# Optimization experiments

Measured on AMD Instinct MI355X. Metric: run time of the kernel, lower is better.

Reference implementation:

```python
import math
import jax, jax.numpy as jnp
import numpy as np

HEAD_DIM = 64


def skew(X):
    # X: (B, M, L). Pad M+1 zeros on last dim, flatten, drop last M, reshape.
    # Shifts row i right by i -> aligns relative positions (adaptive-span trick).
    B, M, L = X.shape
    X = jnp.pad(X, ((0, 0), (0, 0), (0, M + 1)))  # (B, M, L+M+1)
    X = X.reshape(B, -1)[:, :-M].reshape(B, M, M + L)
    return X


def setup_inputs() -> dict:
    key = jax.random.key(0)
    k1, k2, k3, k4 = jax.random.split(key, 4)
    BH, M, D, LIM = 16, 2048, HEAD_DIM, 2048
    return {
        "query": jax.random.normal(k1, (BH, M, D), jnp.float32),
        "key": jax.random.normal(k2, (BH, M, D), jnp.float32),
        "value": jax.random.normal(k3, (BH, M, D), jnp.float32),
        "key_pe": jax.random.normal(k4, (1, D, LIM), jnp.float32),
    }


def reference(query, key, value, key_pe):
    M = query.shape[1]
    Lk = key.shape[1]
    neg_inf = jnp.float32(float("-inf"))
    # causal mask: -inf strictly above diagonal, last M rows
    mask_causal = jnp.triu(jnp.full((Lk, Lk), neg_inf, dtype=query.dtype), k=1)[-M:]
    # content scores: (BH, M, Lk)
    attn = jnp.einsum("bmd,bld->bml", query, key)
    L_size = attn.shape[-1]
    # relative-position scores via skew trick
    attn_pos = jnp.einsum("bmd,xdl->bml", query, key_pe[:, :, -L_size:])
    attn_pos = skew(attn_pos)[:, :, -L_size - 1:-1]
    attn = (attn + attn_pos + mask_causal) / math.sqrt(HEAD_DIM)
    attn = jax.nn.softmax(attn, axis=-1)
    out = jnp.einsum("bml,bld->bmd", attn, value)
    return out  # aux_loss is the constant 0 in the original module
```

## Files before the change

### kernel.cpp

```cpp
#include <hip/hip_runtime.h>
#include <hip/hip_bf16.h>

typedef __attribute__((ext_vector_type(8))) short short8;
typedef __attribute__((ext_vector_type(4))) float f32x4;

#define MFMA16(A, B, C) __builtin_amdgcn_mfma_f32_16x16x32_bf16((A), (B), (C), 0, 0, 0)

#define GL16(gp, lp) __builtin_amdgcn_global_load_lds( \
    (const __attribute__((address_space(1))) void*)(gp), \
    (__attribute__((address_space(3))) void*)(lp), 16, 0, 0)

extern "C" __device__ float __ocml_native_exp2_f32(float);
#define EXP2(x) __ocml_native_exp2_f32(x)

__device__ __forceinline__ unsigned short bfbits(float f) {
  return __builtin_bit_cast(unsigned short, (__bf16)f);
}

constexpr int BH = 16;
constexpr int Mn = 2048;
constexpr int Dn = 64;
constexpr int LIMn = 2048;
constexpr size_t KF_SHORTS = (size_t)BH * 32 * 8 * 512;
constexpr size_t PE_JROWS = 132;
constexpr size_t PEF_SHORTS = PE_JROWS * 2 * 512;
constexpr int PART_SLOT = 4224;
constexpr int SLOTS_PER_HEAD = 72;

__device__ __forceinline__ int part_offs(int mt) {
  return (mt < 16) ? 2 * (mt - 8) : (mt < 24 ? 16 + 3 * (mt - 16) : 40 + 4 * (mt - 24));
}


__global__ void prep_all(const float* __restrict__ K, const float* __restrict__ V,
                         const float* __restrict__ PE,
                         unsigned short* __restrict__ Kf, unsigned short* __restrict__ Vf,
                         unsigned short* __restrict__ PEf) {
  __shared__ float tA[64 * 64];
  __shared__ float tB[64 * 64];
  const int b = blockIdx.x, tid = threadIdx.x;
  const int w = tid >> 6, lane = tid & 63, g = lane >> 4, q15 = lane & 15;

  if (b < 512) {
    const int bh = b >> 5, lt = b & 31;
    const float* Ks = K + ((size_t)bh * Mn + lt * 64) * Dn;
    const float* Vs = V + ((size_t)bh * Mn + lt * 64) * Dn;
    const int row = tid >> 2, c0 = (tid & 3) * 16;
#pragma unroll
    for (int i = 0; i < 4; ++i) {
      *(float4*)&tA[row * 64 + c0 + 4 * i] = ((const float4*)(Ks + (size_t)row * 64 + c0))[i];
      *(float4*)&tB[row * 64 + c0 + 4 * i] = ((const float4*)(Vs + (size_t)row * 64 + c0))[i];
    }
    __syncthreads();
#pragma unroll
    for (int i = 0; i < 2; ++i) {
      const int f = 2 * w + i, nt = f >> 1, s = f & 1;
      short8 uk, uv;
#pragma unroll
      for (int jj = 0; jj < 8; ++jj) {
        uk[jj] = (short)bfbits(tA[(nt * 16 + q15) * 64 + s * 32 + g * 8 + jj]);
        uv[jj] = (short)bfbits(tB[(s * 32 + g * 8 + jj) * 64 + nt * 16 + q15]);
      }
      const size_t base = ((size_t)(bh * 32 + lt) * 8 + f) * 512 + lane * 8;
      *(short8*)&Kf[base] = uk;
      *(short8*)&Vf[base] = uv;
    }
  } else {
    const int pb = b - 512;
    const int c0 = pb * 64;
    const int d = tid >> 2, cc = (tid & 3) * 16;
#pragma unroll
    for (int i = 0; i < 16; ++i) {
      const int cx = c0 + cc + i;
      tA[(cc + i) * 64 + d] = (cx < LIMn) ? PE[(size_t)d * LIMn + cx] : 0.0f;
    }
    __syncthreads();
#pragma unroll
    for (int s = 0; s < 2; ++s) {
      short8 uu;
#pragma unroll
      for (int jj = 0; jj < 8; ++jj)
        uu[jj] = (short)bfbits(tA[(w * 16 + q15) * 64 + s * 32 + g * 8 + jj]);
      *(short8*)&PEf[((size_t)(4 * pb + w) * 2 + s) * 512 + lane * 8] = uu;
    }
  }
}


__launch_bounds__(256)
__global__ void stair_main(const float* __restrict__ Qg,
                           const unsigned short* __restrict__ Kf,
                           const unsigned short* __restrict__ Vf,
                           const unsigned short* __restrict__ PEf,
                           float* __restrict__ Og,
                           float* __restrict__ Part,
                           int split) {
  __shared__ __align__(16) unsigned short Kbuf[2][2][4096];
  __shared__ __align__(16) unsigned short Vbuf[2][2][4096];
  __shared__ __align__(16) unsigned short Plds[4][2048];

  const int tid = threadIdx.x;
  const int w = tid >> 6, lane = tid & 63, g = lane >> 4, q15 = lane & 15;
  const int bid = blockIdx.x;

  int bh, mt, chunk, t0, t1, nch;
  bh = bid & 15;
  if (split) {
    const int u = bid >> 4;
    if (u < 32)      { mt = 31 - (u >> 2); chunk = u & 3; }
    else if (u < 56) { const int v = u - 32, q = v / 3; mt = 23 - q; chunk = v - q * 3; }
    else if (u < 72) { const int v = u - 56; mt = 15 - (v >> 1); chunk = v & 1; }
    else             { mt = 7 - (u - 72); chunk = 0; }
    t0 = chunk * 8;
    t1 = (t0 + 8 < mt + 1) ? (t0 + 8) : (mt + 1);
    nch = (mt + 8) >> 3;
  } else {
    mt = 31 - (bid >> 4); chunk = 0; t0 = 0; t1 = mt + 1; nch = 1;
  }
  const int m0w = mt * 64 + w * 16;
  const int jb0 = 127 - 4 * mt - w;

  const float* Qb = Qg + (size_t)bh * Mn * Dn;
  float* Ob = Og + (size_t)bh * Mn * Dn;

  short8 aq[2];
  {
    const float* qp = Qb + (size_t)(m0w + q15) * Dn;
#pragma unroll
    for (int s = 0; s < 2; ++s) {
      const float4* p = (const float4*)(qp + s * 32 + g * 8);
      float4 f0 = p[0], f1 = p[1];
      short8 a;
      a[0]=(short)bfbits(f0.x); a[1]=(short)bfbits(f0.y); a[2]=(short)bfbits(f0.z); a[3]=(short)bfbits(f0.w);
      a[4]=(short)bfbits(f1.x); a[5]=(short)bfbits(f1.y); a[6]=(short)bfbits(f1.z); a[7]=(short)bfbits(f1.w);
      aq[s] = a;
    }
  }

  float mrun[4], lp[4];
  f32x4 o[4] = {};
#pragma unroll
  for (int r = 0; r < 4; ++r) { mrun[r] = -1e30f; lp[r] = 0.0f; }

  auto STAGE1 = [&](int b, int slot, int t) {
    const size_t toff = ((size_t)(bh * 32 + t) * 8) * 512;
#pragma unroll
    for (int i = 0; i < 2; ++i) {
      const int f = 2 * w + i;
      const size_t off = toff + (size_t)f * 512 + lane * 8;
      GL16(&Kf[off], &Kbuf[b][slot][f * 512]);
      GL16(&Vf[off], &Vbuf[b][slot][f * 512]);
    }
  };

  auto PV = [&](const float sv[4][4], int cur, int slot, int smax) {
#pragma unroll
    for (int nt = 0; nt < 4; ++nt)
#pragma unroll
      for (int r = 0; r < 4; ++r) {
        const int rw = g * 4 + r;
        Plds[w][slot * 1024 + ((rw * 64 + nt * 16 + q15) ^ ((rw & 7) << 3))] = bfbits(sv[nt][r]);
      }
    short8 pa[2];
#pragma unroll
    for (int s = 0; s < 2; ++s)
      if (s <= smax)
        pa[s] = *(short8*)&Plds[w][slot * 1024 + ((q15 * 64 + s * 32 + g * 8) ^ ((q15 & 7) << 3))];
#pragma unroll
    for (int s = 0; s < 2; ++s)
      if (s <= smax)
#pragma unroll
        for (int nt = 0; nt < 4; ++nt) {
          short8 bfr = *(const short8*)&Vbuf[cur][slot][(nt * 2 + s) * 512 + lane * 8];
          o[nt] = MFMA16(pa[s], bfr, o[nt]);
        }
  };

  auto SOFTMAX2 = [&](float svA[4][4], float svB[4][4]) {
    float lmax[4];
#pragma unroll
    for (int r = 0; r < 4; ++r) {
      float a = fmaxf(fmaxf(svA[0][r], svA[1][r]), fmaxf(svA[2][r], svA[3][r]));
      float b = fmaxf(fmaxf(svB[0][r], svB[1][r]), fmaxf(svB[2][r], svB[3][r]));
      lmax[r] = fmaxf(a, b);
    }
    const bool fast = __all((lmax[0] <= mrun[0] + 8.f) & (lmax[1] <= mrun[1] + 8.f) &
                            (lmax[2] <= mrun[2] + 8.f) & (lmax[3] <= mrun[3] + 8.f));
    if (!fast) {
#pragma unroll
      for (int r = 0; r < 4; ++r) {
        float mx = lmax[r];
        mx = fmaxf(mx, __shfl_xor(mx, 1));
        mx = fmaxf(mx, __shfl_xor(mx, 2));
        mx = fmaxf(mx, __shfl_xor(mx, 4));
        mx = fmaxf(mx, __shfl_xor(mx, 8));
        const float mn = fmaxf(mrun[r], mx);
        const float alpha = EXP2((mrun[r] - mn) * 1.44269504f);
        mrun[r] = mn;
        lp[r] *= alpha;
        o[0][r] *= alpha; o[1][r] *= alpha; o[2][r] *= alpha; o[3][r] *= alpha;
      }
    }
#pragma unroll
    for (int nt = 0; nt < 4; ++nt)
#pragma unroll
      for (int r = 0; r < 4; ++r) {
        svA[nt][r] = EXP2((svA[nt][r] - mrun[r]) * 1.44269504f);
        svB[nt][r] = EXP2((svB[nt][r] - mrun[r]) * 1.44269504f);
      }
#pragma unroll
    for (int r = 0; r < 4; ++r)
      lp[r] += ((svA[0][r] + svA[1][r]) + (svA[2][r] + svA[3][r])) +
               ((svB[0][r] + svB[1][r]) + (svB[2][r] + svB[3][r]));
  };

  auto PAIRF = [&](int t, int cur) {
    const int jbA = jb0 + 4 * t;
    const int jbB = jbA + 4;

    short8 peA[2][5], peB[2][5];
#pragma unroll
    for (int s = 0; s < 2; ++s)
#pragma unroll
      for (int uu = 0; uu < 5; ++uu) {
        peA[s][uu] = *(const short8*)&PEf[((size_t)(jbA + uu) * 2 + s) * 512 + lane * 8];
        peB[s][uu] = *(const short8*)&PEf[((size_t)(jbB + uu) * 2 + s) * 512 + lane * 8];
      }

    f32x4 qkA[4] = {}, qkB[4] = {};
#pragma unroll
    for (int s = 0; s < 2; ++s)
#pragma unroll
      for (int nt = 0; nt < 4; ++nt) {
        short8 ba = *(const short8*)&Kbuf[cur][0][(nt * 2 + s) * 512 + lane * 8];
        qkA[nt] = MFMA16(aq[s], ba, qkA[nt]);
        short8 bb = *(const short8*)&Kbuf[cur][1][(nt * 2 + s) * 512 + lane * 8];
        qkB[nt] = MFMA16(aq[s], bb, qkB[nt]);
      }

    f32x4 evA[5] = {};
#pragma unroll
    for (int s = 0; s < 2; ++s)
#pragma unroll
      for (int uu = 0; uu < 5; ++uu) evA[uu] = MFMA16(aq[s], peA[s][uu], evA[uu]);

    float svA[4][4], svB[4][4];
#pragma unroll
    for (int nt = 0; nt < 4; ++nt)
#pragma unroll
      for (int r = 0; r < 4; ++r) {
        const int rw = g * 4 + r;
        const int srcLane = (lane & 48) | ((q15 + 15 - rw) & 15);
        const bool cond = (((q15 + rw + 1) & 15) > rw);
        const float sel = cond ? evA[nt + 1][r] : evA[nt][r];
        svA[nt][r] = (qkA[nt][r] + __shfl(sel, srcLane, 64)) * 0.125f;
      }

    f32x4 evB[5] = {};
#pragma unroll
    for (int s = 0; s < 2; ++s)
#pragma unroll
      for (int uu = 0; uu < 5; ++uu) evB[uu] = MFMA16(aq[s], peB[s][uu], evB[uu]);

#pragma unroll
    for (int nt = 0; nt < 4; ++nt)
#pragma unroll
      for (int r = 0; r < 4; ++r) {
        const int rw = g * 4 + r;
        const int srcLane = (lane & 48) | ((q15 + 15 - rw) & 15);
        const bool cond = (((q15 + rw + 1) & 15) > rw);
        const float sel = cond ? evB[nt + 1][r] : evB[nt][r];
        svB[nt][r] = (qkB[nt][r] + __shfl(sel, srcLane, 64)) * 0.125f;
      }

    SOFTMAX2(svA, svB);
    PV(svA, cur, 0, 1);
    PV(svB, cur, 1, 1);
  };

  auto PAIRD = [&](int t, int cur) {
    const int jbA = jb0 + 4 * t;
    const int jbB = jbA + 4;
    const int ntmaxB = w;
    const int u5B = w + 2;
    const int smaxB = w >> 1;

    short8 peA[2][5], peB[2][5];
#pragma unroll
    for (int s = 0; s < 2; ++s)
#pragma unroll
      for (int uu = 0; uu < 5; ++uu) {
        peA[s][uu] = *(const short8*)&PEf[((size_t)(jbA + uu) * 2 + s) * 512 + lane * 8];
        if (uu < u5B)
          peB[s][uu] = *(const short8*)&PEf[((size_t)(jbB + uu) * 2 + s) * 512 + lane * 8];
      }

    f32x4 qkA[4] = {}, qkB[4] = {};
#pragma unroll
    for (int s = 0; s < 2; ++s)
#pragma unroll
      for (int nt = 0; nt < 4; ++nt) {
        short8 ba = *(const short8*)&Kbuf[cur][0][(nt * 2 + s) * 512 + lane * 8];
        qkA[nt] = MFMA16(aq[s], ba, qkA[nt]);
        if (nt <= ntmaxB) {
          short8 bb = *(const short8*)&Kbuf[cur][1][(nt * 2 + s) * 512 + lane * 8];
          qkB[nt] = MFMA16(aq[s], bb, qkB[nt]);
        }
      }

    f32x4 evA[5] = {};
#pragma unroll
    for (int s = 0; s < 2; ++s)
#pragma unroll
      for (int uu = 0; uu < 5; ++uu) evA[uu] = MFMA16(aq[s], peA[s][uu], evA[uu]);

    float svA[4][4], svB[4][4];
#pragma unroll
    for (int nt = 0; nt < 4; ++nt)
#pragma unroll
      for (int r = 0; r < 4; ++r) {
        const int rw = g * 4 + r;
        const int srcLane = (lane & 48) | ((q15 + 15 - rw) & 15);
        const bool cond = (((q15 + rw + 1) & 15) > rw);
        const float sel = cond ? evA[nt + 1][r] : evA[nt][r];
        svA[nt][r] = (qkA[nt][r] + __shfl(sel, srcLane, 64)) * 0.125f;
        svB[nt][r] = -1e30f;
      }

    f32x4 evB[5] = {};
#pragma unroll
    for (int s = 0; s < 2; ++s)
#pragma unroll
      for (int uu = 0; uu < 5; ++uu)
        if (uu < u5B) evB[uu] = MFMA16(aq[s], peB[s][uu], evB[uu]);

#pragma unroll
    for (int nt = 0; nt < 4; ++nt)
      if (nt <= ntmaxB) {
#pragma unroll
        for (int r = 0; r < 4; ++r) {
          const int rw = g * 4 + r;
          const int srcLane = (lane & 48) | ((q15 + 15 - rw) & 15);
          const bool cond = (((q15 + rw + 1) & 15) > rw);
          const float sel = cond ? evB[nt + 1][r] : evB[nt][r];
          const float er = __shfl(sel, srcLane, 64);
          const int li = nt * 16 + q15;
          const bool masked = (li > w * 16 + rw);
          svB[nt][r] = masked ? -1e30f : (qkB[nt][r] + er) * 0.125f;
        }
      }

    SOFTMAX2(svA, svB);
    PV(svA, cur, 0, 1);
    PV(svB, cur, 1, smaxB);
  };

  auto SINGLE = [&](int t, int cur, bool diag) {
    const int jb = jb0 + 4 * t;
    const int ntmax = diag ? w : 3;
    const int u5 = diag ? (w + 2) : 5;
    const int smax = diag ? (w >> 1) : 1;

    short8 pe[2][5];
#pragma unroll
    for (int s = 0; s < 2; ++s)
#pragma unroll
      for (int uu = 0; uu < 5; ++uu)
        if (uu < u5)
          pe[s][uu] = *(const short8*)&PEf[((size_t)(jb + uu) * 2 + s) * 512 + lane * 8];

    f32x4 qk[4] = {};
#pragma unroll
    for (int s = 0; s < 2; ++s)
#pragma unroll
      for (int nt = 0; nt < 4; ++nt)
        if (nt <= ntmax) {
          short8 bfr = *(const short8*)&Kbuf[cur][0][(nt * 2 + s) * 512 + lane * 8];
          qk[nt] = MFMA16(aq[s], bfr, qk[nt]);
        }
    f32x4 ev[5] = {};
#pragma unroll
    for (int s = 0; s < 2; ++s)
#pragma unroll
      for (int uu = 0; uu < 5; ++uu)
        if (uu < u5) ev[uu] = MFMA16(aq[s], pe[s][uu], ev[uu]);

    float sv[4][4];
#pragma unroll
    for (int nt = 0; nt < 4; ++nt)
#pragma unroll
      for (int r = 0; r < 4; ++r) sv[nt][r] = -1e30f;
#pragma unroll
    for (int nt = 0; nt < 4; ++nt)
      if (nt <= ntmax) {
#pragma unroll
        for (int r = 0; r < 4; ++r) {
          const int rw = g * 4 + r;
          const int srcLane = (lane & 48) | ((q15 + 15 - rw) & 15);
          const bool cond = (((q15 + rw + 1) & 15) > rw);
          const float sel = cond ? ev[nt + 1][r] : ev[nt][r];
          const float er = __shfl(sel, srcLane, 64);
          const int li = nt * 16 + q15;
          const bool masked = diag && (li > w * 16 + rw);
          sv[nt][r] = masked ? -1e30f : (qk[nt][r] + er) * 0.125f;
        }
      }

    float lmax[4];
#pragma unroll
    for (int r = 0; r < 4; ++r)
      lmax[r] = fmaxf(fmaxf(sv[0][r], sv[1][r]), fmaxf(sv[2][r], sv[3][r]));
    const bool fast = __all((lmax[0] <= mrun[0] + 8.f) & (lmax[1] <= mrun[1] + 8.f) &
                            (lmax[2] <= mrun[2] + 8.f) & (lmax[3] <= mrun[3] + 8.f));
    if (!fast) {
#pragma unroll
      for (int r = 0; r < 4; ++r) {
        float mx = lmax[r];
        mx = fmaxf(mx, __shfl_xor(mx, 1));
        mx = fmaxf(mx, __shfl_xor(mx, 2));
        mx = fmaxf(mx, __shfl_xor(mx, 4));
        mx = fmaxf(mx, __shfl_xor(mx, 8));
        const float mn = fmaxf(mrun[r], mx);
        const float alpha = EXP2((mrun[r] - mn) * 1.44269504f);
        mrun[r] = mn;
        lp[r] *= alpha;
        o[0][r] *= alpha; o[1][r] *= alpha; o[2][r] *= alpha; o[3][r] *= alpha;
      }
    }
#pragma unroll
    for (int nt = 0; nt < 4; ++nt)
#pragma unroll
      for (int r = 0; r < 4; ++r)
        sv[nt][r] = EXP2((sv[nt][r] - mrun[r]) * 1.44269504f);
#pragma unroll
    for (int r = 0; r < 4; ++r)
      lp[r] += (sv[0][r] + sv[1][r]) + (sv[2][r] + sv[3][r]);
    PV(sv, cur, 0, smax);
  };

  {
    int cur = 0;
    int t = t0;
    const int n0 = (t1 - t0 >= 2) ? 2 : 1;
    STAGE1(0, 0, t0);
    if (n0 == 2) STAGE1(0, 1, t0 + 1);
    __syncthreads();
    while (t < t1) {
      const int n = (t1 - t >= 2) ? 2 : 1;
      const int rem = t1 - (t + n);
      const int nn = (rem >= 2) ? 2 : rem;
      if (nn > 0) {
        STAGE1(cur ^ 1, 0, t + n);
        if (nn == 2) STAGE1(cur ^ 1, 1, t + n + 1);
      }
      if (n == 2) {
        if (t + 1 == mt) PAIRD(t, cur);
        else PAIRF(t, cur);
      } else {
        SINGLE(t, cur, (t == mt));
      }
      if (nn > 0) __syncthreads();
      cur ^= 1;
      t += n;
    }
  }

  float lr[4];
#pragma unroll
  for (int r = 0; r < 4; ++r) {
    float s = lp[r];
    s += __shfl_xor(s, 1);
    s += __shfl_xor(s, 2);
    s += __shfl_xor(s, 4);
    s += __shfl_xor(s, 8);
    lr[r] = s;
  }

  if (nch == 1) {
#pragma unroll
    for (int nt = 0; nt < 4; ++nt)
#pragma unroll
      for (int r = 0; r < 4; ++r) {
        const int m = m0w + g * 4 + r;
        Ob[(size_t)m * Dn + nt * 16 + q15] = o[nt][r] / lr[r];
      }
  } else {
    float* ps = Part + ((size_t)bh * SLOTS_PER_HEAD + part_offs(mt) + chunk) * PART_SLOT;
#pragma unroll
    for (int nt = 0; nt < 4; ++nt)
#pragma unroll
      for (int r = 0; r < 4; ++r)
        ps[(w * 16 + g * 4 + r) * 64 + nt * 16 + q15] = o[nt][r];
#pragma unroll
    for (int r = 0; r < 4; ++r)
      if (q15 == g * 4 + r) {
        ps[4096 + w * 16 + q15] = mrun[r];
        ps[4160 + w * 16 + q15] = lr[r];
      }
  }
}


__launch_bounds__(256, 4)
__global__ void combine_parts(const float* __restrict__ Part, float* __restrict__ Og) {
  const int bid = blockIdx.x;
  const int bh = bid & 15;
  const int mt = 8 + (bid >> 4);
  const int nch = (mt + 8) >> 3;
  const float* base = Part + ((size_t)bh * SLOTS_PER_HEAD + part_offs(mt)) * PART_SLOT;
  const int tid = threadIdx.x;
  const int row = tid >> 2;
  const int qc = (tid & 3) * 16;

  float mstar = -1e30f;
#pragma unroll
  for (int cc = 0; cc < 4; ++cc)
    if (cc < nch) mstar = fmaxf(mstar, base[cc * PART_SLOT + 4096 + row]);
  float lsum = 0.f;
  f32x4 acc0 = {}, acc1 = {}, acc2 = {}, acc3 = {};
#pragma unroll
  for (int cc = 0; cc < 4; ++cc)
    if (cc < nch) {
      const float* ps = base + cc * PART_SLOT;
      const float sc = EXP2((ps[4096 + row] - mstar) * 1.44269504f);
      lsum += ps[4160 + row] * sc;
      const f32x4* op = (const f32x4*)&ps[row * 64 + qc];
      acc0 += op[0] * sc; acc1 += op[1] * sc; acc2 += op[2] * sc; acc3 += op[3] * sc;
    }
  const float inv = 1.f / lsum;
  float* dst = Og + ((size_t)bh * Mn + mt * 64 + row) * Dn + qc;
  *(f32x4*)&dst[0]  = acc0 * inv;
  *(f32x4*)&dst[4]  = acc1 * inv;
  *(f32x4*)&dst[8]  = acc2 * inv;
  *(f32x4*)&dst[12] = acc3 * inv;
}


constexpr int ESTRIDE = 84;

__launch_bounds__(256, 2)
__global__ void stair_attn_fb(const float* __restrict__ Qg,
                              const float* __restrict__ Kg,
                              const float* __restrict__ Vg,
                              const float* __restrict__ PEg,
                              float* __restrict__ Og) {
  __shared__ __align__(16) unsigned short Kb[64 * 64];
  __shared__ __align__(16) unsigned short Vt[64 * 64];
  __shared__ __align__(16) unsigned short Pb[128 * 64];
  __shared__ __align__(16) float Elds[4 * 16 * ESTRIDE];
  __shared__ __align__(16) unsigned short Plds[4 * 16 * 64];

  const int tid = threadIdx.x;
  const int w = tid >> 6;
  const int lane = tid & 63;
  const int g = lane >> 4;
  const int q15 = lane & 15;

  const int bid = blockIdx.x;
  const int bh = bid & 15;
  const int jid = bid >> 4;
  const int mt = (jid < 16) ? (2 * jid) : (63 - 2 * jid);
  const int m0 = mt * 64;

  const float* Qb = Qg + (size_t)bh * Mn * Dn;
  const float* Kbase = Kg + (size_t)bh * Mn * Dn;
  const float* Vbase = Vg + (size_t)bh * Mn * Dn;
  float* Ob = Og + (size_t)bh * Mn * Dn;

  short8 aq[2];
  {
    const float* qp = Qb + (size_t)(m0 + 16 * w + q15) * Dn;
#pragma unroll
    for (int s = 0; s < 2; ++s) {
      const float4* p = (const float4*)(qp + s * 32 + g * 8);
      float4 f0 = p[0], f1 = p[1];
      short8 a;
      a[0]=(short)bfbits(f0.x); a[1]=(short)bfbits(f0.y); a[2]=(short)bfbits(f0.z); a[3]=(short)bfbits(f0.w);
      a[4]=(short)bfbits(f1.x); a[5]=(short)bfbits(f1.y); a[6]=(short)bfbits(f1.z); a[7]=(short)bfbits(f1.w);
      aq[s] = a;
    }
  }

  float mrun[4], lrun[4];
  f32x4 o[4] = {};
#pragma unroll
  for (int r = 0; r < 4; ++r) { mrun[r] = -1e30f; lrun[r] = 0.0f; }

  const int ntiles = mt + 1;
  const int dso = g * 8;

  for (int t = 0; t < ntiles; ++t) {
    const int l0 = t * 64;
    __syncthreads();
    {
      const int l = tid >> 2;
      const int dq = (tid & 3) * 16;
      const float* kp = Kbase + (size_t)(l0 + l) * Dn + dq;
      short8 u0, u1;
      {
        float4 f = ((const float4*)kp)[0];
        u0[0]=(short)bfbits(f.x); u0[1]=(short)bfbits(f.y); u0[2]=(short)bfbits(f.z); u0[3]=(short)bfbits(f.w);
        f = ((const float4*)kp)[1];
        u0[4]=(short)bfbits(f.x); u0[5]=(short)bfbits(f.y); u0[6]=(short)bfbits(f.z); u0[7]=(short)bfbits(f.w);
        f = ((const float4*)kp)[2];
        u1[0]=(short)bfbits(f.x); u1[1]=(short)bfbits(f.y); u1[2]=(short)bfbits(f.z); u1[3]=(short)bfbits(f.w);
        f = ((const float4*)kp)[3];
        u1[4]=(short)bfbits(f.x); u1[5]=(short)bfbits(f.y); u1[6]=(short)bfbits(f.z); u1[7]=(short)bfbits(f.w);
      }
      const int swz = (l & 7) << 3;
      *(short8*)&Kb[(l * 64 + dq) ^ swz] = u0;
      *(short8*)&Kb[(l * 64 + dq + 8) ^ swz] = u1;
    }
    {
      const int lrow = lane;
      const int ds = w * 16;
      const float* vp = Vbase + (size_t)(l0 + lrow) * Dn + ds;
#pragma unroll
      for (int i = 0; i < 4; ++i) {
        float4 f = ((const float4*)vp)[i];
        int c0 = ds + 4 * i;
        Vt[((c0 + 0) * 64 + lrow) ^ (((c0 + 0) & 7) << 3)] = bfbits(f.x);
        Vt[((c0 + 1) * 64 + lrow) ^ (((c0 + 1) & 7) << 3)] = bfbits(f.y);
        Vt[((c0 + 2) * 64 + lrow) ^ (((c0 + 2) & 7) << 3)] = bfbits(f.z);
        Vt[((c0 + 3) * 64 + lrow) ^ (((c0 + 3) & 7) << 3)] = bfbits(f.w);
      }
    }
    {
      const int d = lane;
      const int cc = w * 32;
      const int cb = (2048 - 64) - m0 + l0;
      const float* pp = PEg + (size_t)d * LIMn + (cb + cc);
      if (cb + cc + 31 < LIMn) {
#pragma unroll
        for (int i = 0; i < 8; ++i) {
          float4 f = ((const float4*)pp)[i];
          int c0 = cc + 4 * i;
          Pb[((c0 + 0) * 64 + d) ^ (((c0 + 0) & 7) << 3)] = bfbits(f.x);
          Pb[((c0 + 1) * 64 + d) ^ (((c0 + 1) & 7) << 3)] = bfbits(f.y);
          Pb[((c0 + 2) * 64 + d) ^ (((c0 + 2) & 7) << 3)] = bfbits(f.z);
          Pb[((c0 + 3) * 64 + d) ^ (((c0 + 3) & 7) << 3)] = bfbits(f.w);
        }
      } else {
        for (int i = 0; i < 32; ++i) {
          int cabs = cb + cc + i;
          float f = (cabs < LIMn) ? pp[i] : 0.0f;
          int c0 = cc + i;
          Pb[(c0 * 64 + d) ^ ((c0 & 7) << 3)] = bfbits(f);
        }
      }
    }
    __syncthreads();

    f32x4 qk[4] = {};
#pragma unroll
    for (int s = 0; s < 2; ++s)
#pragma unroll
      for (int nt = 0; nt < 4; ++nt) {
        int l = nt * 16 + q15;
        short8 b = *(short8*)&Kb[(l * 64 + s * 32 + dso) ^ ((l & 7) << 3)];
        qk[nt] = MFMA16(aq[s], b, qk[nt]);
      }

    f32x4 ev[5] = {};
    const int ntb = 3 - w;
#pragma unroll
    for (int s = 0; s < 2; ++s)
#pragma unroll
      for (int u5 = 0; u5 < 5; ++u5) {
        int c = (ntb + u5) * 16 + q15;
        short8 b = *(short8*)&Pb[(c * 64 + s * 32 + dso) ^ ((c & 7) << 3)];
        ev[u5] = MFMA16(aq[s], b, ev[u5]);
      }
    float* Ew = Elds + w * 16 * ESTRIDE;
#pragma unroll
    for (int u5 = 0; u5 < 5; ++u5)
#pragma unroll
      for (int r = 0; r < 4; ++r)
        Ew[(g * 4 + r) * ESTRIDE + u5 * 16 + q15] = ev[u5][r];

    const bool diag = (t == ntiles - 1);
    float sv[4][4];
#pragma unroll
    for (int nt = 0; nt < 4; ++nt) {
      int li = nt * 16 + q15;
#pragma unroll
      for (int r = 0; r < 4; ++r) {
        int rw = g * 4 + r;
        float eread = Ew[rw * ESTRIDE + (15 - rw + li)];
        bool masked = diag && (li > (16 * w + rw));
        sv[nt][r] = masked ? -1e30f : (qk[nt][r] + eread) * 0.125f;
      }
    }

    float mnew[4], alpha[4];
#pragma unroll
    for (int r = 0; r < 4; ++r) {
      float mx = fmaxf(fmaxf(sv[0][r], sv[1][r]), fmaxf(sv[2][r], sv[3][r]));
      mx = fmaxf(mx, __shfl_xor(mx, 1));
      mx = fmaxf(mx, __shfl_xor(mx, 2));
      mx = fmaxf(mx, __shfl_xor(mx, 4));
      mx = fmaxf(mx, __shfl_xor(mx, 8));
      float mn = fmaxf(mrun[r], mx);
      alpha[r] = exp2f((mrun[r] - mn) * 1.44269504f);
      mnew[r] = mn;
      mrun[r] = mn;
    }
    float pexp[4][4];
#pragma unroll
    for (int nt = 0; nt < 4; ++nt)
#pragma unroll
      for (int r = 0; r < 4; ++r)
        pexp[nt][r] = exp2f((sv[nt][r] - mnew[r]) * 1.44269504f);
#pragma unroll
    for (int r = 0; r < 4; ++r) {
      float sum = (pexp[0][r] + pexp[1][r]) + (pexp[2][r] + pexp[3][r]);
      sum += __shfl_xor(sum, 1);
      sum += __shfl_xor(sum, 2);
      sum += __shfl_xor(sum, 4);
      sum += __shfl_xor(sum, 8);
      lrun[r] = lrun[r] * alpha[r] + sum;
      o[0][r] *= alpha[r];
      o[1][r] *= alpha[r];
      o[2][r] *= alpha[r];
      o[3][r] *= alpha[r];
    }

    unsigned short* Pw = Plds + w * 16 * 64;
#pragma unroll
    for (int nt = 0; nt < 4; ++nt)
#pragma unroll
      for (int r = 0; r < 4; ++r) {
        int rw = g * 4 + r;
        Pw[(rw * 64 + nt * 16 + q15) ^ ((rw & 7) << 3)] = bfbits(pexp[nt][r]);
      }
    short8 pa[2];
#pragma unroll
    for (int s = 0; s < 2; ++s)
      pa[s] = *(short8*)&Pw[(q15 * 64 + s * 32 + dso) ^ ((q15 & 7) << 3)];

#pragma unroll
    for (int s = 0; s < 2; ++s)
#pragma unroll
      for (int nt = 0; nt < 4; ++nt) {
        int d = nt * 16 + q15;
        short8 b = *(short8*)&Vt[(d * 64 + s * 32 + dso) ^ ((d & 7) << 3)];
        o[nt] = MFMA16(pa[s], b, o[nt]);
      }
  }

#pragma unroll
  for (int nt = 0; nt < 4; ++nt)
#pragma unroll
    for (int r = 0; r < 4; ++r) {
      int m = m0 + 16 * w + g * 4 + r;
      Ob[(size_t)m * Dn + nt * 16 + q15] = o[nt][r] / lrun[r];
    }
}


extern "C" void kernel_launch(void* const* d_in, const int* in_sizes, int n_in,
                              void* d_out, int out_size, void* d_ws, size_t ws_size,
                              hipStream_t stream) {
  (void)in_sizes; (void)n_in; (void)out_size;
  const float* Q  = (const float*)d_in[0];
  const float* K  = (const float*)d_in[1];
  const float* V  = (const float*)d_in[2];
  const float* PE = (const float*)d_in[3];
  float* Out = (float*)d_out;

  const size_t szK = KF_SHORTS * sizeof(unsigned short);
  const size_t szV = szK;
  const size_t szP = PEF_SHORTS * sizeof(unsigned short);
  const size_t szPart = (size_t)BH * SLOTS_PER_HEAD * PART_SLOT * 4;
  const size_t need1 = szK + szV + szP;
  const size_t need2 = need1 + szPart;

  if (ws_size >= need1) {
    unsigned short* Kf  = (unsigned short*)d_ws;
    unsigned short* Vf  = (unsigned short*)((char*)d_ws + szK);
    unsigned short* PEf = (unsigned short*)((char*)d_ws + szK + szV);
    float* Part = (float*)((char*)d_ws + need1);

    hipLaunchKernelGGL(prep_all, dim3(512 + 33), dim3(256), 0, stream, K, V, PE, Kf, Vf, PEf);
    if (ws_size >= need2) {
      hipLaunchKernelGGL(stair_main, dim3(BH * 80), dim3(256), 0, stream,
                         Q, Kf, Vf, PEf, Out, Part, 1);
      hipLaunchKernelGGL(combine_parts, dim3(BH * 24), dim3(256), 0, stream, Part, Out);
    } else {
      hipLaunchKernelGGL(stair_main, dim3(512), dim3(256), 0, stream,
                         Q, Kf, Vf, PEf, Out, (float*)d_ws, 0);
    }
  } else {
    hipLaunchKernelGGL(stair_attn_fb, dim3(512), dim3(256), 0, stream, Q, K, V, PE, Out);
  }
}
```

Measured before the change: 66.87 us.

## Fold softmax scale into Q, single-buffer V in LDS, shrink P scratch

Pre-multiplies Q by 0.125*log2(e) before the bf16 conversion, which removes the per-score scale and per-exp multiply and rescales the max-threshold to match. V is no longer double-buffered: it is loaded per step into one LDS buffer and waited on with an explicit vmcnt(0) before the PV MFMAs. The P staging area is cut to a 16x40 padded tile per half, and LDS use drops overall, which may allow more blocks per CU. The cost is that V loads are exposed within each step rather than prefetched a full iteration ahead, and the vmcnt(0) wait also drains the in-flight K prefetch.

```diff
diff --git a/kernel.cpp b/kernel.cpp
--- a/kernel.cpp
+++ b/kernel.cpp
@@ -26,6 +26,8 @@
 constexpr size_t PEF_SHORTS = PE_JROWS * 2 * 512;
 constexpr int PART_SLOT = 4224;
 constexpr int SLOTS_PER_HEAD = 72;
+constexpr float QSCALE = 0.125f * 1.44269504f;
+constexpr float THR = 11.5409504f;
 
 __device__ __forceinline__ int part_offs(int mt) {
   return (mt < 16) ? 2 * (mt - 8) : (mt < 24 ? 16 + 3 * (mt - 16) : 40 + 4 * (mt - 24));
@@ -96,8 +98,8 @@
                            float* __restrict__ Part,
                            int split) {
   __shared__ __align__(16) unsigned short Kbuf[2][2][4096];
-  __shared__ __align__(16) unsigned short Vbuf[2][2][4096];
-  __shared__ __align__(16) unsigned short Plds[4][2048];
+  __shared__ __align__(16) unsigned short Vbuf[2][4096];
+  __shared__ __align__(16) unsigned short Plds[4][640];
 
   const int tid = threadIdx.x;
   const int w = tid >> 6, lane = tid & 63, g = lane >> 4, q15 = lane & 15;
@@ -122,6 +124,7 @@
 
   const float* Qb = Qg + (size_t)bh * Mn * Dn;
   float* Ob = Og + (size_t)bh * Mn * Dn;
+  unsigned short* Pw = Plds[w];
 
   short8 aq[2];
   {
@@ -131,8 +134,10 @@
       const float4* p = (const float4*)(qp + s * 32 + g * 8);
       float4 f0 = p[0], f1 = p[1];
       short8 a;
-      a[0]=(short)bfbits(f0.x); a[1]=(short)bfbits(f0.y); a[2]=(short)bfbits(f0.z); a[3]=(short)bfbits(f0.w);
-      a[4]=(short)bfbits(f1.x); a[5]=(short)bfbits(f1.y); a[6]=(short)bfbits(f1.z); a[7]=(short)bfbits(f1.w);
+      a[0]=(short)bfbits(f0.x*QSCALE); a[1]=(short)bfbits(f0.y*QSCALE);
+      a[2]=(short)bfbits(f0.z*QSCALE); a[3]=(short)bfbits(f0.w*QSCALE);
+      a[4]=(short)bfbits(f1.x*QSCALE); a[5]=(short)bfbits(f1.y*QSCALE);
+      a[6]=(short)bfbits(f1.z*QSCALE); a[7]=(short)bfbits(f1.w*QSCALE);
       aq[s] = a;
     }
   }
@@ -142,36 +147,41 @@
 #pragma unroll
   for (int r = 0; r < 4; ++r) { mrun[r] = -1e30f; lp[r] = 0.0f; }
 
-  auto STAGE1 = [&](int b, int slot, int t) {
+  auto STAGEK = [&](int b, int slot, int t) {
     const size_t toff = ((size_t)(bh * 32 + t) * 8) * 512;
 #pragma unroll
     for (int i = 0; i < 2; ++i) {
       const int f = 2 * w + i;
-      const size_t off = toff + (size_t)f * 512 + lane * 8;
-      GL16(&Kf[off], &Kbuf[b][slot][f * 512]);
-      GL16(&Vf[off], &Vbuf[b][slot][f * 512]);
+      GL16(&Kf[toff + (size_t)f * 512 + lane * 8], &Kbuf[b][slot][f * 512]);
     }
   };
-
-  auto PV = [&](const float sv[4][4], int cur, int slot, int smax) {
-#pragma unroll
-    for (int nt = 0; nt < 4; ++nt)
-#pragma unroll
-      for (int r = 0; r < 4; ++r) {
-        const int rw = g * 4 + r;
-        Plds[w][slot * 1024 + ((rw * 64 + nt * 16 + q15) ^ ((rw & 7) << 3))] = bfbits(sv[nt][r]);
-      }
+  auto STAGEV = [&](int slot, int t) {
+    const size_t toff = ((size_t)(bh * 32 + t) * 8) * 512;
+#pragma unroll
+    for (int i = 0; i < 2; ++i) {
+      const int f = 2 * w + i;
+      GL16(&Vf[toff + (size_t)f * 512 + lane * 8], &Vbuf[slot][f * 512]);
+    }
+  };
+
+  auto PV = [&](const float sv[4][4], int slot, int smax) {
     short8 pa[2];
 #pragma unroll
+    for (int h = 0; h < 2; ++h)
+      if (h <= smax) {
+#pragma unroll
+        for (int nt2 = 0; nt2 < 2; ++nt2)
+#pragma unroll
+          for (int r = 0; r < 4; ++r)
+            Pw[(g * 4 + r) * 40 + nt2 * 16 + q15] = bfbits(sv[2 * h + nt2][r]);
+        pa[h] = *(short8*)&Pw[q15 * 40 + g * 8];
+      }
+#pragma unroll
     for (int s = 0; s < 2; ++s)
       if (s <= smax)
-        pa[s] = *(short8*)&Plds[w][slot * 1024 + ((q15 * 64 + s * 32 + g * 8) ^ ((q15 & 7) << 3))];
-#pragma unroll
-    for (int s = 0; s < 2; ++s)
-      if (s <= smax)
 #pragma unroll
         for (int nt = 0; nt < 4; ++nt) {
-          short8 bfr = *(const short8*)&Vbuf[cur][slot][(nt * 2 + s) * 512 + lane * 8];
+          short8 bfr = *(const short8*)&Vbuf[slot][(nt * 2 + s) * 512 + lane * 8];
           o[nt] = MFMA16(pa[s], bfr, o[nt]);
         }
   };
@@ -184,8 +194,8 @@
       float b = fmaxf(fmaxf(svB[0][r], svB[1][r]), fmaxf(svB[2][r], svB[3][r]));
       lmax[r] = fmaxf(a, b);
     }
-    const bool fast = __all((lmax[0] <= mrun[0] + 8.f) & (lmax[1] <= mrun[1] + 8.f) &
-                            (lmax[2] <= mrun[2] + 8.f) & (lmax[3] <= mrun[3] + 8.f));
+    const bool fast = __all((lmax[0] <= mrun[0] + THR) & (lmax[1] <= mrun[1] + THR) &
+                            (lmax[2] <= mrun[2] + THR) & (lmax[3] <= mrun[3] + THR));
     if (!fast) {
 #pragma unroll
       for (int r = 0; r < 4; ++r) {
@@ -195,7 +205,7 @@
         mx = fmaxf(mx, __shfl_xor(mx, 4));
         mx = fmaxf(mx, __shfl_xor(mx, 8));
         const float mn = fmaxf(mrun[r], mx);
-        const float alpha = EXP2((mrun[r] - mn) * 1.44269504f);
+        const float alpha = EXP2(mrun[r] - mn);
         mrun[r] = mn;
         lp[r] *= alpha;
         o[0][r] *= alpha; o[1][r] *= alpha; o[2][r] *= alpha; o[3][r] *= alpha;
@@ -205,8 +215,8 @@
     for (int nt = 0; nt < 4; ++nt)
 #pragma unroll
       for (int r = 0; r < 4; ++r) {
-        svA[nt][r] = EXP2((svA[nt][r] - mrun[r]) * 1.44269504f);
-        svB[nt][r] = EXP2((svB[nt][r] - mrun[r]) * 1.44269504f);
+        svA[nt][r] = EXP2(svA[nt][r] - mrun[r]);
+        svB[nt][r] = EXP2(svB[nt][r] - mrun[r]);
       }
 #pragma unroll
     for (int r = 0; r < 4; ++r)
@@ -253,7 +263,7 @@
         const int srcLane = (lane & 48) | ((q15 + 15 - rw) & 15);
         const bool cond = (((q15 + rw + 1) & 15) > rw);
         const float sel = cond ? evA[nt + 1][r] : evA[nt][r];
-        svA[nt][r] = (qkA[nt][r] + __shfl(sel, srcLane, 64)) * 0.125f;
+        svA[nt][r] = qkA[nt][r] + __shfl(sel, srcLane, 64);
       }
 
     f32x4 evB[5] = {};
@@ -270,12 +280,13 @@
         const int srcLane = (lane & 48) | ((q15 + 15 - rw) & 15);
         const bool cond = (((q15 + rw + 1) & 15) > rw);
         const float sel = cond ? evB[nt + 1][r] : evB[nt][r];
-        svB[nt][r] = (qkB[nt][r] + __shfl(sel, srcLane, 64)) * 0.125f;
+        svB[nt][r] = qkB[nt][r] + __shfl(sel, srcLane, 64);
       }
 
     SOFTMAX2(svA, svB);
-    PV(svA, cur, 0, 1);
-    PV(svB, cur, 1, 1);
+    asm volatile("s_waitcnt vmcnt(0)" ::: "memory");
+    PV(svA, 0, 1);
+    PV(svB, 1, 1);
   };
 
   auto PAIRD = [&](int t, int cur) {
@@ -323,7 +334,7 @@
         const int srcLane = (lane & 48) | ((q15 + 15 - rw) & 15);
         const bool cond = (((q15 + rw + 1) & 15) > rw);
         const float sel = cond ? evA[nt + 1][r] : evA[nt][r];
-        svA[nt][r] = (qkA[nt][r] + __shfl(sel, srcLane, 64)) * 0.125f;
+        svA[nt][r] = qkA[nt][r] + __shfl(sel, srcLane, 64);
         svB[nt][r] = -1e30f;
       }
 
@@ -346,13 +357,14 @@
           const float er = __shfl(sel, srcLane, 64);
           const int li = nt * 16 + q15;
           const bool masked = (li > w * 16 + rw);
-          svB[nt][r] = masked ? -1e30f : (qkB[nt][r] + er) * 0.125f;
+          svB[nt][r] = masked ? -1e30f : (qkB[nt][r] + er);
         }
       }
 
     SOFTMAX2(svA, svB);
-    PV(svA, cur, 0, 1);
-    PV(svB, cur, 1, smaxB);
+    asm volatile("s_waitcnt vmcnt(0)" ::: "memory");
+    PV(svA, 0, 1);
+    PV(svB, 1, smaxB);
   };
 
   auto SINGLE = [&](int t, int cur, bool diag) {
@@ -402,7 +414,7 @@
           const float er = __shfl(sel, srcLane, 64);
           const int li = nt * 16 + q15;
           const bool masked = diag && (li > w * 16 + rw);
-          sv[nt][r] = masked ? -1e30f : (qk[nt][r] + er) * 0.125f;
+          sv[nt][r] = masked ? -1e30f : (qk[nt][r] + er);
         }
       }
 
@@ -410,8 +422,8 @@
 #pragma unroll
     for (int r = 0; r < 4; ++r)
       lmax[r] = fmaxf(fmaxf(sv[0][r], sv[1][r]), fmaxf(sv[2][r], sv[3][r]));
-    const bool fast = __all((lmax[0] <= mrun[0] + 8.f) & (lmax[1] <= mrun[1] + 8.f) &
-                            (lmax[2] <= mrun[2] + 8.f) & (lmax[3] <= mrun[3] + 8.f));
+    const bool fast = __all((lmax[0] <= mrun[0] + THR) & (lmax[1] <= mrun[1] + THR) &
+                            (lmax[2] <= mrun[2] + THR) & (lmax[3] <= mrun[3] + THR));
     if (!fast) {
 #pragma unroll
       for (int r = 0; r < 4; ++r) {
@@ -421,7 +433,7 @@
         mx = fmaxf(mx, __shfl_xor(mx, 4));
         mx = fmaxf(mx, __shfl_xor(mx, 8));
         const float mn = fmaxf(mrun[r], mx);
-        const float alpha = EXP2((mrun[r] - mn) * 1.44269504f);
+        const float alpha = EXP2(mrun[r] - mn);
         mrun[r] = mn;
         lp[r] *= alpha;
         o[0][r] *= alpha; o[1][r] *= alpha; o[2][r] *= alpha; o[3][r] *= alpha;
@@ -431,27 +443,30 @@
     for (int nt = 0; nt < 4; ++nt)
 #pragma unroll
       for (int r = 0; r < 4; ++r)
-        sv[nt][r] = EXP2((sv[nt][r] - mrun[r]) * 1.44269504f);
+        sv[nt][r] = EXP2(sv[nt][r] - mrun[r]);
 #pragma unroll
     for (int r = 0; r < 4; ++r)
       lp[r] += (sv[0][r] + sv[1][r]) + (sv[2][r] + sv[3][r]);
-    PV(sv, cur, 0, smax);
+    asm volatile("s_waitcnt vmcnt(0)" ::: "memory");
+    PV(sv, 0, smax);
   };
 
   {
     int cur = 0;
     int t = t0;
     const int n0 = (t1 - t0 >= 2) ? 2 : 1;
-    STAGE1(0, 0, t0);
-    if (n0 == 2) STAGE1(0, 1, t0 + 1);
+    STAGEK(0, 0, t0);
+    if (n0 == 2) STAGEK(0, 1, t0 + 1);
     __syncthreads();
     while (t < t1) {
       const int n = (t1 - t >= 2) ? 2 : 1;
+      STAGEV(0, t);
+      if (n == 2) STAGEV(1, t + 1);
       const int rem = t1 - (t + n);
       const int nn = (rem >= 2) ? 2 : rem;
       if (nn > 0) {
-        STAGE1(cur ^ 1, 0, t + n);
-        if (nn == 2) STAGE1(cur ^ 1, 1, t + n + 1);
+        STAGEK(cur ^ 1, 0, t + n);
+        if (nn == 2) STAGEK(cur ^ 1, 1, t + n + 1);
       }
       if (n == 2) {
         if (t + 1 == mt) PAIRD(t, cur);
@@ -522,7 +537,7 @@
   for (int cc = 0; cc < 4; ++cc)
     if (cc < nch) {
       const float* ps = base + cc * PART_SLOT;
-      const float sc = EXP2((ps[4096 + row] - mstar) * 1.44269504f);
+      const float sc = EXP2(ps[4096 + row] - mstar);
       lsum += ps[4160 + row] * sc;
       const f32x4* op = (const f32x4*)&ps[row * 64 + qc];
       acc0 += op[0] * sc; acc1 += op[1] * sc; acc2 += op[2] * sc; acc3 += op[3] * sc;
```

Measured after the change: 65.44 us, median of 2. 2.1% less time.
